# Performance work log

Measured on AMD Instinct MI355X. Metric: run time of the kernel, lower is better.

Reference implementation:

```python
import jax, jax.numpy as jnp
import numpy as np

B, L, D, H = 2, 2048, 1024, 16
HD = D // H  # head dim = 64


def setup_inputs() -> dict:
    key = jax.random.key(0)
    ks = jax.random.split(key, 5)
    s = 1.0 / np.sqrt(D)
    return {
        "x": jax.random.normal(ks[0], (B, L, D), dtype=jnp.float32),
        "mask": jnp.ones((B, 1, 1, L), dtype=jnp.int32),
        "Wq": jax.random.normal(ks[1], (D, D), dtype=jnp.float32) * s,
        "bq": jnp.zeros((D,), dtype=jnp.float32),
        "Wk": jax.random.normal(ks[2], (D, D), dtype=jnp.float32) * s,
        "bk": jnp.zeros((D,), dtype=jnp.float32),
        "Wv": jax.random.normal(ks[3], (D, D), dtype=jnp.float32) * s,
        "bv": jnp.zeros((D,), dtype=jnp.float32),
        "Wo": jax.random.normal(ks[4], (D, D), dtype=jnp.float32) * s,
        "bo": jnp.zeros((D,), dtype=jnp.float32),
    }


def reference(x, mask, Wq, bq, Wk, bk, Wv, bv, Wo, bo):
    Bx, Lx = x.shape[0], x.shape[1]
    # torch nn.Linear: y = x @ W.T + b
    q = (jnp.einsum("bld,ed->ble", x, Wq) + bq).reshape(Bx, Lx, H, HD).transpose(0, 2, 1, 3)
    k = (jnp.einsum("bld,ed->ble", x, Wk) + bk).reshape(Bx, Lx, H, HD).transpose(0, 2, 1, 3)
    v = (jnp.einsum("bld,ed->ble", x, Wv) + bv).reshape(Bx, Lx, H, HD).transpose(0, 2, 1, 3)
    # [B, H, L, L] scores
    scores = jnp.einsum("bhqd,bhkd->bhqk", q, k) / np.sqrt(HD).astype(np.float32)
    # faithful to original: masked positions are set to the tiny value 1e-9 (not -inf)
    scores = jnp.where(mask == 0, jnp.float32(1e-9), scores)
    attn = jax.nn.softmax(scores, axis=-1)
    # dropout_prob=0.0 -> identity (eval mode)
    out = jnp.einsum("bhqk,bhkd->bhqd", attn, v)  # [B, H, L, HD]
    out = out.transpose(0, 2, 1, 3).reshape(Bx, Lx, D)
    return jnp.einsum("bld,ed->ble", out, Wo) + bo
```

## Files before the change

kernel.cpp:

```cpp
#include <hip/hip_runtime.h>
#include <hip/hip_bf16.h>

typedef _Float16 f16;
typedef _Float16 f16x8 __attribute__((ext_vector_type(8)));
typedef _Float16 f16x4 __attribute__((ext_vector_type(4)));
typedef float f32x4 __attribute__((ext_vector_type(4)));

#define LDS_LOAD16(gptr, lptr)                                                             \
  __builtin_amdgcn_global_load_lds(                                                        \
      (const __attribute__((address_space(1))) unsigned int*)(gptr),                       \
      (__attribute__((address_space(3))) unsigned int*)(lptr), 16, 0, 0)

#define ALPHA 0.18033688f
#define MASKVAL (1.44269504e-9f - 8.0f)

__global__ __launch_bounds__(256) void conv_all(const float* __restrict__ x,
                                                const float* __restrict__ Wq,
                                                const float* __restrict__ Wk,
                                                const float* __restrict__ Wv,
                                                const float* __restrict__ Wo,
                                                f16* __restrict__ xh, f16* __restrict__ wqh,
                                                f16* __restrict__ wkh, f16* __restrict__ wvh,
                                                f16* __restrict__ woh) {
  int i = blockIdx.x * 256 + threadIdx.x;
  const float* src;
  f16* dst;
  int off;
  if (i < 524288) {
    src = x; dst = xh; off = i;
  } else {
    int j = i - 524288;
    int w = j >> 17;
    off = j & 131071;
    src = (w == 0) ? Wq : (w == 1) ? Wk : (w == 2) ? Wv : Wo;
    dst = (w == 0) ? wqh : (w == 1) ? wkh : (w == 2) ? wvh : woh;
  }
  const float4* s4 = (const float4*)src;
  float4 a = s4[2 * off];
  float4 b = s4[2 * off + 1];
  f16x8 o = {(f16)a.x, (f16)a.y, (f16)a.z, (f16)a.w,
             (f16)b.x, (f16)b.y, (f16)b.z, (f16)b.w};
  *(f16x8*)(dst + (size_t)off * 8) = o;
}

__global__ __launch_bounds__(256) void gemm_qkv(const f16* __restrict__ A,
                                                const f16* __restrict__ W0,
                                                const f16* __restrict__ W1,
                                                const f16* __restrict__ W2,
                                                const float* __restrict__ b0,
                                                const float* __restrict__ b1,
                                                const float* __restrict__ b2,
                                                f16* __restrict__ qo, f16* __restrict__ ko,
                                                f16* __restrict__ vo) {
  constexpr int K = 1024, BM = 128, BK = 32;
  __shared__ f16 aT[BM * BK];
  __shared__ f16 bT[BM * BK];
  const int z = blockIdx.z;
  const f16* Bw = (z == 0) ? W0 : (z == 1) ? W1 : W2;
  const float* bias = (z == 0) ? b0 : (z == 1) ? b1 : b2;
  const int tid = threadIdx.x, wid = tid >> 6, lane = tid & 63;
  const int mb = blockIdx.y * BM, nb = blockIdx.x * BM;
  const int wr = wid >> 1, wc = wid & 1;
  const int lr = lane & 15, hi = lane >> 4;

  f32x4 acc[4][4] = {};

  const int r0 = tid >> 2, s0 = tid & 3;
  const int ci1 = 256 + tid, r1 = ci1 >> 2, s1 = ci1 & 3;

  for (int kt = 0; kt < K / BK; ++kt) {
    __syncthreads();
    const int kb = kt * BK;
    LDS_LOAD16(A + (size_t)(mb + r0) * K + kb + s0 * 8, (char*)aT + wid * 1024);
    LDS_LOAD16(Bw + (size_t)(nb + r0) * K + kb + s0 * 8, (char*)bT + wid * 1024);
    LDS_LOAD16(A + (size_t)(mb + r1) * K + kb + s1 * 8, (char*)aT + 4096 + wid * 1024);
    LDS_LOAD16(Bw + (size_t)(nb + r1) * K + kb + s1 * 8, (char*)bT + 4096 + wid * 1024);
    __syncthreads();

    f16x8 af[4], bf[4];
#pragma unroll
    for (int i = 0; i < 4; ++i) af[i] = *(const f16x8*)&aT[(wr * 64 + i * 16 + lr) * BK + hi * 8];
#pragma unroll
    for (int j = 0; j < 4; ++j) bf[j] = *(const f16x8*)&bT[(wc * 64 + j * 16 + lr) * BK + hi * 8];
    __builtin_amdgcn_s_setprio(1);
#pragma unroll
    for (int i = 0; i < 4; ++i)
#pragma unroll
      for (int j = 0; j < 4; ++j)
        acc[i][j] = __builtin_amdgcn_mfma_f32_16x16x32_f16(af[i], bf[j], acc[i][j], 0, 0, 0);
    __builtin_amdgcn_s_setprio(0);
  }

  const float scale = (z == 0) ? ALPHA : 1.0f;
#pragma unroll
  for (int i = 0; i < 4; ++i) {
#pragma unroll
    for (int j = 0; j < 4; ++j) {
      const int row = mb + wr * 64 + i * 16 + hi * 4;
      const int col = nb + wc * 64 + j * 16 + lr;
      const float bv = bias[col];
      const int hh = col >> 6, dd = col & 63;
      if (z == 2) {
        const int bb = row >> 11, l = row & 2047;
        f16x4 v4;
#pragma unroll
        for (int r = 0; r < 4; ++r) v4[r] = (f16)(acc[i][j][r] + bv);
        *(f16x4*)(vo + ((((size_t)bb * 16 + hh) * 64 + dd) * 2048 + l)) = v4;
      } else {
        f16* o = z ? ko : qo;
#pragma unroll
        for (int r = 0; r < 4; ++r) {
          const int m2 = row + r;
          const int bb = m2 >> 11, l = m2 & 2047;
          o[((((size_t)bb * 16 + hh) * 2048 + l) * 64) + dd] = (f16)((acc[i][j][r] + bv) * scale);
        }
      }
    }
  }
}

__global__ __launch_bounds__(256) void gemm_o(const f16* __restrict__ A,
                                              const f16* __restrict__ W,
                                              const float* __restrict__ bias,
                                              float* __restrict__ out) {
  constexpr int K = 1024, N = 1024, BK = 32;
  __shared__ f16 aT[64 * BK];
  __shared__ f16 bT[128 * BK];
  const int tid = threadIdx.x, wid = tid >> 6, lane = tid & 63;
  const int lr = lane & 15, hi = lane >> 4;
  const int mb = blockIdx.y * 64, nb = blockIdx.x * 128;
  const int wr = wid >> 1, wc = wid & 1;
  f32x4 acc[2][4] = {};
  const int ra = tid >> 2, sa = tid & 3;
  const int rb1 = (256 + tid) >> 2, sb1 = (256 + tid) & 3;

  for (int kt = 0; kt < K / BK; ++kt) {
    __syncthreads();
    const int kb = kt * BK;
    LDS_LOAD16(A + (size_t)(mb + ra) * K + kb + sa * 8, (char*)aT + wid * 1024);
    LDS_LOAD16(W + (size_t)(nb + ra) * K + kb + sa * 8, (char*)bT + wid * 1024);
    LDS_LOAD16(W + (size_t)(nb + rb1) * K + kb + sb1 * 8, (char*)bT + 4096 + wid * 1024);
    __syncthreads();
    f16x8 af[2], bf[4];
#pragma unroll
    for (int i = 0; i < 2; ++i) af[i] = *(const f16x8*)&aT[(wr * 32 + i * 16 + lr) * BK + hi * 8];
#pragma unroll
    for (int j = 0; j < 4; ++j) bf[j] = *(const f16x8*)&bT[(wc * 64 + j * 16 + lr) * BK + hi * 8];
    __builtin_amdgcn_s_setprio(1);
#pragma unroll
    for (int i = 0; i < 2; ++i)
#pragma unroll
      for (int j = 0; j < 4; ++j)
        acc[i][j] = __builtin_amdgcn_mfma_f32_16x16x32_f16(af[i], bf[j], acc[i][j], 0, 0, 0);
    __builtin_amdgcn_s_setprio(0);
  }
#pragma unroll
  for (int i = 0; i < 2; ++i)
#pragma unroll
    for (int j = 0; j < 4; ++j) {
      const int col = nb + wc * 64 + j * 16 + lr;
      const float bv = bias[col];
#pragma unroll
      for (int r = 0; r < 4; ++r)
        out[(size_t)(mb + wr * 32 + i * 16 + hi * 4 + r) * N + col] = acc[i][j][r] + bv;
    }
}

__global__ __launch_bounds__(128) void attn2w(const f16* __restrict__ Qh,
                                              const f16* __restrict__ Kh,
                                              const f16* __restrict__ Vt,
                                              const int* __restrict__ mask,
                                              f16* __restrict__ Oa) {
  constexpr int L = 2048, HD = 64, H = 16, NT = L / 64;
  __shared__ f16 kT[2][64 * 64];
  __shared__ f16 vT[2][64 * 64];
  __shared__ f16 pT[2][32 * 64];

  const int tid = threadIdx.x, w = tid >> 6, lane = tid & 63;
  const int lr = lane & 15, hi = lane >> 4;
  const int sw = lr & 7;

  const int bid = blockIdx.x;
  const int head = (bid & 7) * 4 + (bid >> 8);
  const int qb = (bid >> 3) & 31;
  const int b = head >> 4, h = head & 15;
  const int qr0 = qb * 64 + w * 32;

  const f16* Qb = Qh + (size_t)head * L * HD;
  const f16* Kb = Kh + (size_t)head * L * HD;
  const f16* Vb = Vt + (size_t)head * HD * L;
  const int* mrow = mask + b * L;

  const int srow = lane >> 3;
  const int schk = (lane & 7) ^ srow;
  char* kTb = (char*)kT;
  char* vTb = (char*)vT;
  char* pTb = (char*)pT + w * 4096;

#define STAGE2W(bb, kt)                                                                     \
  _Pragma("unroll") for (int c = 0; c < 4; ++c) {                                           \
    LDS_LOAD16(Kb + (size_t)((kt) * 64 + w * 32 + c * 8 + srow) * HD + schk * 8,            \
               kTb + (bb) * 8192 + w * 4096 + c * 1024);                                    \
    LDS_LOAD16(Vb + (size_t)(w * 32 + c * 8 + srow) * L + (kt) * 64 + schk * 8,             \
               vTb + (bb) * 8192 + w * 4096 + c * 1024);                                    \
  }

  f16x8 qf[2][2];
#pragma unroll
  for (int qg = 0; qg < 2; ++qg)
#pragma unroll
    for (int k2 = 0; k2 < 2; ++k2)
      qf[qg][k2] = *(const f16x8*)&Qb[(size_t)(qr0 + qg * 16 + lr) * HD + k2 * 32 + hi * 8];

  f32x4 oacc[2][4] = {};
  f32x4 lacc[2] = {};
  const f16x8 ones = {1, 1, 1, 1, 1, 1, 1, 1};

  int4 mvA[4], mvB[4];
#pragma unroll
  for (int nf = 0; nf < 4; ++nf) mvA[nf] = *(const int4*)&mrow[nf * 16 + hi * 4];
  STAGE2W(0, 0);

#define ATTN_ITER(kt, MVR, MVL)                                                             \
  do {                                                                                      \
    asm volatile("s_waitcnt vmcnt(0)" ::: "memory");                                        \
    __builtin_amdgcn_s_barrier();                                                           \
    if ((kt) + 1 < NT) {                                                                    \
      _Pragma("unroll") for (int nf = 0; nf < 4; ++nf)                                      \
          MVL[nf] = *(const int4*)&mrow[((kt) + 1) * 64 + nf * 16 + hi * 4];                \
      STAGE2W(((kt) + 1) & 1, (kt) + 1);                                                    \
    }                                                                                       \
    const char* kB = kTb + ((kt) & 1) * 8192;                                               \
    const char* vB = vTb + ((kt) & 1) * 8192;                                               \
    f16x8 kf[4][2];                                                                         \
    _Pragma("unroll") for (int nf = 0; nf < 4; ++nf)                                        \
        _Pragma("unroll") for (int k2 = 0; k2 < 2; ++k2)                                    \
            kf[nf][k2] = *(const f16x8*)(kB + (nf * 16 + lr) * 128 + ((k2 * 4 + hi) ^ sw) * 16); \
    f32x4 s[2][4];                                                                          \
    __builtin_amdgcn_s_setprio(1);                                                          \
    _Pragma("unroll") for (int qg = 0; qg < 2; ++qg)                                        \
        _Pragma("unroll") for (int nf = 0; nf < 4; ++nf) {                                  \
      f32x4 z = {-8.f, -8.f, -8.f, -8.f};                                                   \
      z = __builtin_amdgcn_mfma_f32_16x16x32_f16(kf[nf][0], qf[qg][0], z, 0, 0, 0);         \
      z = __builtin_amdgcn_mfma_f32_16x16x32_f16(kf[nf][1], qf[qg][1], z, 0, 0, 0);         \
      s[qg][nf] = z;                                                                        \
    }                                                                                       \
    __builtin_amdgcn_s_setprio(0);                                                          \
    _Pragma("unroll") for (int qg = 0; qg < 2; ++qg)                                        \
        _Pragma("unroll") for (int nf = 0; nf < 4; ++nf) {                                  \
      float p0 = __builtin_amdgcn_exp2f(MVR[nf].x ? s[qg][nf][0] : MASKVAL);                \
      float p1 = __builtin_amdgcn_exp2f(MVR[nf].y ? s[qg][nf][1] : MASKVAL);                \
      float p2 = __builtin_amdgcn_exp2f(MVR[nf].z ? s[qg][nf][2] : MASKVAL);                \
      float p3 = __builtin_amdgcn_exp2f(MVR[nf].w ? s[qg][nf][3] : MASKVAL);                \
      f16x4 pw = {(f16)p0, (f16)p1, (f16)p2, (f16)p3};                                      \
      *(f16x4*)(pTb + (qg * 16 + lr) * 128 + ((nf * 32 + hi * 8) ^ (sw << 4))) = pw;        \
    }                                                                                       \
    asm volatile("s_waitcnt lgkmcnt(0)" ::: "memory");                                      \
    __builtin_amdgcn_sched_barrier(0);                                                      \
    f16x8 pf[2][2];                                                                         \
    _Pragma("unroll") for (int qg = 0; qg < 2; ++qg)                                        \
        _Pragma("unroll") for (int k2 = 0; k2 < 2; ++k2)                                    \
            pf[qg][k2] = *(const f16x8*)(pTb + (qg * 16 + lr) * 128 + ((k2 * 4 + hi) ^ sw) * 16); \
    __builtin_amdgcn_s_setprio(1);                                                          \
    _Pragma("unroll") for (int k2 = 0; k2 < 2; ++k2) {                                      \
      _Pragma("unroll") for (int df = 0; df < 4; ++df) {                                    \
        f16x8 vf = *(const f16x8*)(vB + (df * 16 + lr) * 128 + ((k2 * 4 + hi) ^ sw) * 16);  \
        oacc[0][df] = __builtin_amdgcn_mfma_f32_16x16x32_f16(pf[0][k2], vf, oacc[0][df], 0, 0, 0); \
        oacc[1][df] = __builtin_amdgcn_mfma_f32_16x16x32_f16(pf[1][k2], vf, oacc[1][df], 0, 0, 0); \
      }                                                                                     \
      lacc[0] = __builtin_amdgcn_mfma_f32_16x16x32_f16(pf[0][k2], ones, lacc[0], 0, 0, 0);  \
      lacc[1] = __builtin_amdgcn_mfma_f32_16x16x32_f16(pf[1][k2], ones, lacc[1], 0, 0, 0);  \
    }                                                                                       \
    __builtin_amdgcn_s_setprio(0);                                                          \
  } while (0)

  for (int kt = 0; kt < NT; kt += 2) {
    ATTN_ITER(kt, mvA, mvB);
    ATTN_ITER(kt + 1, mvB, mvA);
  }

#pragma unroll
  for (int qg = 0; qg < 2; ++qg) {
    f32x4 rinv;
#pragma unroll
    for (int r = 0; r < 4; ++r) rinv[r] = 1.0f / lacc[qg][r];
#pragma unroll
    for (int df = 0; df < 4; ++df)
#pragma unroll
      for (int r = 0; r < 4; ++r) {
        const int l = qr0 + qg * 16 + hi * 4 + r;
        Oa[(((size_t)b * L + l) * H + h) * HD + df * 16 + lr] = (f16)(oacc[qg][df][r] * rinv[r]);
      }
  }
}

extern "C" void kernel_launch(void* const* d_in, const int* in_sizes, int n_in,
                              void* d_out, int out_size, void* d_ws, size_t ws_size,
                              hipStream_t stream) {
  const float* x  = (const float*)d_in[0];
  const int* mask = (const int*)d_in[1];
  const float* Wq = (const float*)d_in[2];
  const float* bq = (const float*)d_in[3];
  const float* Wk = (const float*)d_in[4];
  const float* bk = (const float*)d_in[5];
  const float* Wv = (const float*)d_in[6];
  const float* bv = (const float*)d_in[7];
  const float* Wo = (const float*)d_in[8];
  const float* bo = (const float*)d_in[9];
  float* out = (float*)d_out;

  char* ws = (char*)d_ws;
  const size_t MB = 1u << 20;
  f16* xh  = (f16*)(ws);
  f16* wqh = (f16*)(ws + 8 * MB);
  f16* wkh = (f16*)(ws + 10 * MB);
  f16* wvh = (f16*)(ws + 12 * MB);
  f16* woh = (f16*)(ws + 14 * MB);
  f16* qh  = (f16*)(ws + 16 * MB);
  f16* kh  = (f16*)(ws + 24 * MB);
  f16* vth = (f16*)(ws + 32 * MB);
  f16* oah = (f16*)(ws + 40 * MB);

  conv_all<<<4096, 256, 0, stream>>>(x, Wq, Wk, Wv, Wo, xh, wqh, wkh, wvh, woh);

  gemm_qkv<<<dim3(8, 32, 3), 256, 0, stream>>>(xh, wqh, wkh, wvh, bq, bk, bv, qh, kh, vth);

  attn2w<<<dim3(1024), 128, 0, stream>>>(qh, kh, vth, mask, oah);

  gemm_o<<<dim3(8, 64), 256, 0, stream>>>(oah, woh, bo, out);
}
```

Before: 126.3 us.

## Shuffle P fragments in registers instead of LDS round-trip, fast-path all-ones mask

Replaces the LDS write and read-back of the softmax probability tile with an in-register transpose built from v_permlane32_swap and ds_swizzle, removing the LDS store, lgkmcnt wait and reload. The mask is checked once per block, and if every entry is set the per-tile mask loads and selects are skipped. It also drops the -8 score offset, now starting the QK accumulator at zero, merges the LDS buffers into one array with precomputed swizzled base pointers, and sets launch bounds to 2 blocks per SM. The register shuffle adds cross-lane ops and depends on lane-mapping correctness, and removing the -8 offset changes the exponent range fed to exp2.

```diff
diff --git a/kernel.cpp b/kernel.cpp
--- a/kernel.cpp
+++ b/kernel.cpp
@@ -4,7 +4,9 @@
 typedef _Float16 f16;
 typedef _Float16 f16x8 __attribute__((ext_vector_type(8)));
 typedef _Float16 f16x4 __attribute__((ext_vector_type(4)));
+typedef _Float16 f16x2 __attribute__((ext_vector_type(2)));
 typedef float f32x4 __attribute__((ext_vector_type(4)));
+typedef int i32x4 __attribute__((ext_vector_type(4)));
 
 #define LDS_LOAD16(gptr, lptr)                                                             \
   __builtin_amdgcn_global_load_lds(                                                        \
@@ -12,7 +14,7 @@
       (__attribute__((address_space(3))) unsigned int*)(lptr), 16, 0, 0)
 
 #define ALPHA 0.18033688f
-#define MASKVAL (1.44269504e-9f - 8.0f)
+#define MASKVAL 1.44269504e-9f
 
 __global__ __launch_bounds__(256) void conv_all(const float* __restrict__ x,
                                                 const float* __restrict__ Wq,
@@ -166,19 +168,18 @@
     }
 }
 
-__global__ __launch_bounds__(128) void attn2w(const f16* __restrict__ Qh,
-                                              const f16* __restrict__ Kh,
-                                              const f16* __restrict__ Vt,
-                                              const int* __restrict__ mask,
-                                              f16* __restrict__ Oa) {
+__global__ __launch_bounds__(128, 2) void attn2w(const f16* __restrict__ Qh,
+                                                 const f16* __restrict__ Kh,
+                                                 const f16* __restrict__ Vt,
+                                                 const int* __restrict__ mask,
+                                                 f16* __restrict__ Oa) {
   constexpr int L = 2048, HD = 64, H = 16, NT = L / 64;
-  __shared__ f16 kT[2][64 * 64];
-  __shared__ f16 vT[2][64 * 64];
-  __shared__ f16 pT[2][32 * 64];
+  __shared__ __align__(16) char ldsb[32768];
 
   const int tid = threadIdx.x, w = tid >> 6, lane = tid & 63;
   const int lr = lane & 15, hi = lane >> 4;
   const int sw = lr & 7;
+  const bool oddhi = (hi & 1) != 0;
 
   const int bid = blockIdx.x;
   const int head = (bid & 7) * 4 + (bid >> 8);
@@ -191,19 +192,30 @@
   const f16* Vb = Vt + (size_t)head * HD * L;
   const int* mrow = mask + b * L;
 
+  int mred = 1;
+  {
+    const int4* m4 = (const int4*)mrow;
+#pragma unroll
+    for (int j = 0; j < 8; ++j) {
+      int4 v = m4[lane + j * 64];
+      mred &= v.x & v.y & v.z & v.w;
+    }
+  }
+  const bool allm = __all(mred == 1);
+
   const int srow = lane >> 3;
   const int schk = (lane & 7) ^ srow;
-  char* kTb = (char*)kT;
-  char* vTb = (char*)vT;
-  char* pTb = (char*)pT + w * 4096;
 
 #define STAGE2W(bb, kt)                                                                     \
   _Pragma("unroll") for (int c = 0; c < 4; ++c) {                                           \
     LDS_LOAD16(Kb + (size_t)((kt) * 64 + w * 32 + c * 8 + srow) * HD + schk * 8,            \
-               kTb + (bb) * 8192 + w * 4096 + c * 1024);                                    \
+               ldsb + (bb) * 16384 + w * 4096 + c * 1024);                                  \
     LDS_LOAD16(Vb + (size_t)(w * 32 + c * 8 + srow) * L + (kt) * 64 + schk * 8,             \
-               vTb + (bb) * 8192 + w * 4096 + c * 1024);                                    \
-  }
+               ldsb + (bb) * 16384 + 8192 + w * 4096 + c * 1024);                           \
+  }
+
+  const char* kbase0 = ldsb + lr * 128 + ((hi ^ sw) * 16);
+  const char* kbase1 = ldsb + lr * 128 + (((4 + hi) ^ sw) * 16);
 
   f16x8 qf[2][2];
 #pragma unroll
@@ -214,57 +226,83 @@
 
   f32x4 oacc[2][4] = {};
   f32x4 lacc[2] = {};
+  const f32x4 zacc = {0.f, 0.f, 0.f, 0.f};
   const f16x8 ones = {1, 1, 1, 1, 1, 1, 1, 1};
 
   int4 mvA[4], mvB[4];
-#pragma unroll
-  for (int nf = 0; nf < 4; ++nf) mvA[nf] = *(const int4*)&mrow[nf * 16 + hi * 4];
+  if (!allm) {
+#pragma unroll
+    for (int nf = 0; nf < 4; ++nf) mvA[nf] = *(const int4*)&mrow[nf * 16 + hi * 4];
+  }
   STAGE2W(0, 0);
 
-#define ATTN_ITER(kt, MVR, MVL)                                                             \
+#define ATTN_ITER(kt, P, MVR, MVL)                                                          \
   do {                                                                                      \
     asm volatile("s_waitcnt vmcnt(0)" ::: "memory");                                        \
     __builtin_amdgcn_s_barrier();                                                           \
     if ((kt) + 1 < NT) {                                                                    \
-      _Pragma("unroll") for (int nf = 0; nf < 4; ++nf)                                      \
-          MVL[nf] = *(const int4*)&mrow[((kt) + 1) * 64 + nf * 16 + hi * 4];                \
-      STAGE2W(((kt) + 1) & 1, (kt) + 1);                                                    \
-    }                                                                                       \
-    const char* kB = kTb + ((kt) & 1) * 8192;                                               \
-    const char* vB = vTb + ((kt) & 1) * 8192;                                               \
+      if (!allm) {                                                                          \
+        _Pragma("unroll") for (int nf = 0; nf < 4; ++nf)                                    \
+            MVL[nf] = *(const int4*)&mrow[((kt) + 1) * 64 + nf * 16 + hi * 4];              \
+      }                                                                                     \
+      STAGE2W((P) ^ 1, (kt) + 1);                                                           \
+    }                                                                                       \
     f16x8 kf[4][2];                                                                         \
-    _Pragma("unroll") for (int nf = 0; nf < 4; ++nf)                                        \
-        _Pragma("unroll") for (int k2 = 0; k2 < 2; ++k2)                                    \
-            kf[nf][k2] = *(const f16x8*)(kB + (nf * 16 + lr) * 128 + ((k2 * 4 + hi) ^ sw) * 16); \
+    _Pragma("unroll") for (int nf = 0; nf < 4; ++nf) {                                      \
+      kf[nf][0] = *(const f16x8*)(kbase0 + (P) * 16384 + nf * 2048);                        \
+      kf[nf][1] = *(const f16x8*)(kbase1 + (P) * 16384 + nf * 2048);                        \
+    }                                                                                       \
     f32x4 s[2][4];                                                                          \
     __builtin_amdgcn_s_setprio(1);                                                          \
     _Pragma("unroll") for (int qg = 0; qg < 2; ++qg)                                        \
         _Pragma("unroll") for (int nf = 0; nf < 4; ++nf) {                                  \
-      f32x4 z = {-8.f, -8.f, -8.f, -8.f};                                                   \
-      z = __builtin_amdgcn_mfma_f32_16x16x32_f16(kf[nf][0], qf[qg][0], z, 0, 0, 0);         \
-      z = __builtin_amdgcn_mfma_f32_16x16x32_f16(kf[nf][1], qf[qg][1], z, 0, 0, 0);         \
-      s[qg][nf] = z;                                                                        \
+      f32x4 z = __builtin_amdgcn_mfma_f32_16x16x32_f16(kf[nf][0], qf[qg][0], zacc, 0, 0, 0);\
+      s[qg][nf] = __builtin_amdgcn_mfma_f32_16x16x32_f16(kf[nf][1], qf[qg][1], z, 0, 0, 0); \
     }                                                                                       \
     __builtin_amdgcn_s_setprio(0);                                                          \
-    _Pragma("unroll") for (int qg = 0; qg < 2; ++qg)                                        \
-        _Pragma("unroll") for (int nf = 0; nf < 4; ++nf) {                                  \
-      float p0 = __builtin_amdgcn_exp2f(MVR[nf].x ? s[qg][nf][0] : MASKVAL);                \
-      float p1 = __builtin_amdgcn_exp2f(MVR[nf].y ? s[qg][nf][1] : MASKVAL);                \
-      float p2 = __builtin_amdgcn_exp2f(MVR[nf].z ? s[qg][nf][2] : MASKVAL);                \
-      float p3 = __builtin_amdgcn_exp2f(MVR[nf].w ? s[qg][nf][3] : MASKVAL);                \
-      f16x4 pw = {(f16)p0, (f16)p1, (f16)p2, (f16)p3};                                      \
-      *(f16x4*)(pTb + (qg * 16 + lr) * 128 + ((nf * 32 + hi * 8) ^ (sw << 4))) = pw;        \
-    }                                                                                       \
-    asm volatile("s_waitcnt lgkmcnt(0)" ::: "memory");                                      \
-    __builtin_amdgcn_sched_barrier(0);                                                      \
     f16x8 pf[2][2];                                                                         \
-    _Pragma("unroll") for (int qg = 0; qg < 2; ++qg)                                        \
-        _Pragma("unroll") for (int k2 = 0; k2 < 2; ++k2)                                    \
-            pf[qg][k2] = *(const f16x8*)(pTb + (qg * 16 + lr) * 128 + ((k2 * 4 + hi) ^ sw) * 16); \
+    _Pragma("unroll") for (int qg = 0; qg < 2; ++qg) {                                      \
+      int wpk[4][2];                                                                        \
+      _Pragma("unroll") for (int nf = 0; nf < 4; ++nf) {                                    \
+        float p0, p1, p2, p3;                                                               \
+        if (allm) {                                                                         \
+          p0 = __builtin_amdgcn_exp2f(s[qg][nf][0]);                                        \
+          p1 = __builtin_amdgcn_exp2f(s[qg][nf][1]);                                        \
+          p2 = __builtin_amdgcn_exp2f(s[qg][nf][2]);                                        \
+          p3 = __builtin_amdgcn_exp2f(s[qg][nf][3]);                                        \
+        } else {                                                                            \
+          p0 = __builtin_amdgcn_exp2f(MVR[nf].x ? s[qg][nf][0] : MASKVAL);                  \
+          p1 = __builtin_amdgcn_exp2f(MVR[nf].y ? s[qg][nf][1] : MASKVAL);                  \
+          p2 = __builtin_amdgcn_exp2f(MVR[nf].z ? s[qg][nf][2] : MASKVAL);                  \
+          p3 = __builtin_amdgcn_exp2f(MVR[nf].w ? s[qg][nf][3] : MASKVAL);                  \
+        }                                                                                   \
+        f16x2 h0 = {(f16)p0, (f16)p1};                                                      \
+        f16x2 h1 = {(f16)p2, (f16)p3};                                                      \
+        wpk[nf][0] = __builtin_bit_cast(int, h0);                                           \
+        wpk[nf][1] = __builtin_bit_cast(int, h1);                                           \
+      }                                                                                     \
+      _Pragma("unroll") for (int k2 = 0; k2 < 2; ++k2) {                                    \
+        int A0 = wpk[2 * k2][0], B0 = wpk[2 * k2 + 1][0];                                   \
+        int A1 = wpk[2 * k2][1], B1 = wpk[2 * k2 + 1][1];                                   \
+        asm("v_permlane32_swap_b32 %0, %1" : "+v"(A0), "+v"(B0));                           \
+        asm("v_permlane32_swap_b32 %0, %1" : "+v"(A1), "+v"(B1));                           \
+        int SA0 = __builtin_amdgcn_ds_swizzle(A0, 0x401F);                                  \
+        int SB0 = __builtin_amdgcn_ds_swizzle(B0, 0x401F);                                  \
+        int SA1 = __builtin_amdgcn_ds_swizzle(A1, 0x401F);                                  \
+        int SB1 = __builtin_amdgcn_ds_swizzle(B1, 0x401F);                                  \
+        int c0 = oddhi ? SB0 : A0;                                                          \
+        int c1 = oddhi ? SB1 : A1;                                                          \
+        int c2 = oddhi ? B0 : SA0;                                                          \
+        int c3 = oddhi ? B1 : SA1;                                                          \
+        i32x4 cc = {c0, c1, c2, c3};                                                        \
+        pf[qg][k2] = __builtin_bit_cast(f16x8, cc);                                         \
+      }                                                                                     \
+    }                                                                                       \
     __builtin_amdgcn_s_setprio(1);                                                          \
     _Pragma("unroll") for (int k2 = 0; k2 < 2; ++k2) {                                      \
+      const char* vbase = (k2 ? kbase1 : kbase0) + (P) * 16384 + 8192;                      \
       _Pragma("unroll") for (int df = 0; df < 4; ++df) {                                    \
-        f16x8 vf = *(const f16x8*)(vB + (df * 16 + lr) * 128 + ((k2 * 4 + hi) ^ sw) * 16);  \
+        f16x8 vf = *(const f16x8*)(vbase + df * 2048);                                      \
         oacc[0][df] = __builtin_amdgcn_mfma_f32_16x16x32_f16(pf[0][k2], vf, oacc[0][df], 0, 0, 0); \
         oacc[1][df] = __builtin_amdgcn_mfma_f32_16x16x32_f16(pf[1][k2], vf, oacc[1][df], 0, 0, 0); \
       }                                                                                     \
@@ -275,8 +313,8 @@
   } while (0)
 
   for (int kt = 0; kt < NT; kt += 2) {
-    ATTN_ITER(kt, mvA, mvB);
-    ATTN_ITER(kt + 1, mvB, mvA);
+    ATTN_ITER(kt, 0, mvA, mvB);
+    ATTN_ITER(kt + 1, 1, mvB, mvA);
   }
 
 #pragma unroll
```

Result: faster. 118.7 us (-6.1%).
